# Optimization experiments

Hardware: AMD Instinct MI355X
Metric: run time of the kernel (lower is better)

Reference implementation:

```python
import jax, jax.numpy as jnp
import numpy as np

TEMPERATURE = 0.07
NUM_UNIFY_CLASSES = 256


def setup_inputs() -> dict:
    key = jax.random.key(0)
    k1, k2, k3 = jax.random.split(key, 3)
    b, c, h, w = 16, 256, 128, 128
    # small-magnitude feats so exp(logits) stays finite at temperature 0.07
    feats = jax.random.normal(k1, (b, c, h, w), dtype=jnp.float32) * 0.05
    queue = jax.random.normal(k2, (NUM_UNIFY_CLASSES, c), dtype=jnp.float32)
    queue = queue / jnp.linalg.norm(queue, axis=1, keepdims=True)  # unit rows, as a memory bank would hold
    labels = jax.random.randint(k3, (b * h * w, NUM_UNIFY_CLASSES), 0, 2, dtype=jnp.int32)
    return {"feats": feats, "queue": queue, "labels": labels}


def reference(feats, queue, labels):
    b, c, h, w = feats.shape
    # [b,c,h,w] -> [N, c]
    f = jnp.transpose(feats, (0, 2, 3, 1)).reshape(-1, c)
    # [N, M] logits
    logits = (f @ queue.T) / TEMPERATURE
    pos_mask = labels.reshape(-1, NUM_UNIFY_CLASSES).astype(logits.dtype)
    neg_mask = 1.0 - pos_mask
    sum_neg = jnp.sum(jnp.exp(logits) * neg_mask, axis=1)   # [N]
    sum_pos = jnp.sum(jnp.exp(-logits) * pos_mask, axis=1)  # [N]
    loss = jnp.log(sum_neg * sum_pos + 1.0)                 # [N]
    lb_num = jnp.sum(loss != 0)
    return jnp.where(lb_num == 0, jnp.float32(0.0),
                     jnp.sum(loss) / jnp.maximum(lb_num, 1).astype(loss.dtype))
```

## Files before the change

### kernel.cpp

```cpp
#include <hip/hip_runtime.h>
#include <hip/hip_bf16.h>


typedef __bf16 bf16x8 __attribute__((ext_vector_type(8)));
typedef float floatx4 __attribute__((ext_vector_type(4)));

using gl_void = const __attribute__((address_space(1))) void;
using lds_void = __attribute__((address_space(3))) void;

union BFrag {
  unsigned int u32[4];
  bf16x8 bf;
};

__device__ __forceinline__ unsigned int pack_bf2(float a, float b) {
  unsigned int ua = __float_as_uint(a) + 0x8000u;
  unsigned int ub = __float_as_uint(b) + 0x8000u;
  return (ua >> 16) | (ub & 0xffff0000u);
}

__global__ void qprep(const float* __restrict__ queue,
                      unsigned short* __restrict__ qs,
                      float* __restrict__ accum) {
  const int gt = blockIdx.x * 256 + threadIdx.x;
  const int t = gt >> 6;
  const int lane = gt & 63;
  const int m = ((t >> 3) << 4) | (lane & 15);
  const int k0 = ((t & 7) << 5) | ((lane >> 4) << 3);
  const float* qr = queue + m * 256 + k0;
  const float TINV = 14.2857142857142857f;
  BFrag u;
#pragma unroll
  for (int j = 0; j < 4; ++j)
    u.u32[j] = pack_bf2(qr[2 * j] * TINV, qr[2 * j + 1] * TINV);
  *(uint4*)(qs + (size_t)gt * 8) = *(const uint4*)u.u32;
  if (gt == 0) { accum[0] = 0.0f; accum[1] = 0.0f; }
}

__global__ __launch_bounds__(256, 2) void pcl_main(
    const float* __restrict__ feats,
    const int* __restrict__ labels,
    const unsigned short* __restrict__ qs,
    float* __restrict__ accum) {
  __shared__ float Fl[16640];
  __shared__ float Red[8][64];

  const int bx = blockIdx.x;
  const int bidx = bx >> 8;
  const int hw0 = (bx & 255) << 6;
  const int tid = threadIdx.x;
  const int w = tid >> 6;
  const int lane = tid & 63;
  const int qd = lane >> 4;
  const int s = lane & 15;

  {
    const float* gbase = feats + (size_t)bidx * 256 * 16384 + hw0;
#pragma unroll
    for (int i = 0; i < 16; ++i) {
      const int g = (w << 4) + i;
      const float* gp = gbase + (size_t)((g << 2) + qd) * 16384 + (s << 2);
      float* lp = &Fl[g * 260];
      __builtin_amdgcn_global_load_lds((gl_void*)gp, (lds_void*)lp, 16, 0, 0);
    }
  }

  floatx4 acc[4][4];
#pragma unroll
  for (int mt = 0; mt < 4; ++mt)
#pragma unroll
    for (int nt = 0; nt < 4; ++nt)
      acc[mt][nt] = floatx4{0.0f, 0.0f, 0.0f, 0.0f};

  __syncthreads();

  const bf16x8* qfrag = (const bf16x8*)qs;
#pragma unroll
  for (int ks = 0; ks < 8; ++ks) {
    bf16x8 af[4];
#pragma unroll
    for (int mt = 0; mt < 4; ++mt) {
      const int t = ((((w << 2) + mt) << 3) | ks);
      af[mt] = qfrag[t * 64 + lane];
    }
    bf16x8 bfv[4];
#pragma unroll
    for (int nt = 0; nt < 4; ++nt) {
      const float* bp = &Fl[((ks << 3) + (qd << 1)) * 260 + (nt << 4) + s];
      BFrag u;
      u.u32[0] = pack_bf2(bp[0], bp[64]);
      u.u32[1] = pack_bf2(bp[128], bp[192]);
      u.u32[2] = pack_bf2(bp[260], bp[324]);
      u.u32[3] = pack_bf2(bp[388], bp[452]);
      bfv[nt] = u.bf;
    }
#pragma unroll
    for (int mt = 0; mt < 4; ++mt)
#pragma unroll
      for (int nt = 0; nt < 4; ++nt)
        acc[mt][nt] = __builtin_amdgcn_mfma_f32_16x16x32_bf16(af[mt], bfv[nt],
                                                              acc[mt][nt], 0, 0, 0);
  }

  const size_t nbase = (size_t)bx << 6;
  int4 lab[4][4];
#pragma unroll
  for (int mt = 0; mt < 4; ++mt)
#pragma unroll
    for (int nt = 0; nt < 4; ++nt)
      lab[mt][nt] = *(const int4*)(labels + ((nbase + (nt << 4) + s) << 8) +
                                   (w << 6) + (mt << 4) + (qd << 2));

  float nn[4] = {0.f, 0.f, 0.f, 0.f};
  float pp[4] = {0.f, 0.f, 0.f, 0.f};
#define ACCUM_TERM(LV, AV)                          \
  do {                                              \
    const float fl_ = (float)(LV);                  \
    const float l_ = (AV);                          \
    const float e_ = __expf(l_);                    \
    const float en_ = __expf(-l_);                  \
    nn[nt] += (1.0f - fl_) * e_;                    \
    pp[nt] += fl_ * en_;                            \
  } while (0)

#pragma unroll
  for (int mt = 0; mt < 4; ++mt) {
#pragma unroll
    for (int nt = 0; nt < 4; ++nt) {
      const int4 lb = lab[mt][nt];
      const floatx4 a = acc[mt][nt];
      ACCUM_TERM(lb.x, a[0]);
      ACCUM_TERM(lb.y, a[1]);
      ACCUM_TERM(lb.z, a[2]);
      ACCUM_TERM(lb.w, a[3]);
    }
  }
#undef ACCUM_TERM

#pragma unroll
  for (int nt = 0; nt < 4; ++nt) {
    nn[nt] += __shfl_xor(nn[nt], 16);
    nn[nt] += __shfl_xor(nn[nt], 32);
    pp[nt] += __shfl_xor(pp[nt], 16);
    pp[nt] += __shfl_xor(pp[nt], 32);
  }
  if (lane < 16) {
#pragma unroll
    for (int nt = 0; nt < 4; ++nt) {
      Red[(w << 1) | 0][(nt << 4) + lane] = nn[nt];
      Red[(w << 1) | 1][(nt << 4) + lane] = pp[nt];
    }
  }
  __syncthreads();

  if (tid < 64) {
    const float sn = Red[0][tid] + Red[2][tid] + Red[4][tid] + Red[6][tid];
    const float sp = Red[1][tid] + Red[3][tid] + Red[5][tid] + Red[7][tid];
    float loss = logf(sn * sp + 1.0f);
    float c = (loss != 0.0f) ? 1.0f : 0.0f;
#pragma unroll
    for (int off = 32; off > 0; off >>= 1) {
      loss += __shfl_xor(loss, off);
      c += __shfl_xor(c, off);
    }
    if (tid == 0) {
      atomicAdd(&accum[0], loss);
      atomicAdd(&accum[1], c);
    }
  }
}

__global__ void pcl_finalize(const float* __restrict__ accum,
                             float* __restrict__ out) {
  const float ssum = accum[0];
  const float c = accum[1];
  out[0] = (c != 0.0f) ? (ssum / c) : 0.0f;
}

extern "C" void kernel_launch(void* const* d_in, const int* in_sizes, int n_in,
                              void* d_out, int out_size, void* d_ws, size_t ws_size,
                              hipStream_t stream) {
  (void)in_sizes; (void)n_in; (void)out_size; (void)ws_size;
  const float* feats = (const float*)d_in[0];
  const float* queue = (const float*)d_in[1];
  const int* labels = (const int*)d_in[2];

  unsigned short* qs = (unsigned short*)d_ws;
  float* accum = (float*)((char*)d_ws + 256 * 256 * sizeof(unsigned short));

  qprep<<<32, 256, 0, stream>>>(queue, qs, accum);
  pcl_main<<<4096, 256, 0, stream>>>(feats, labels, qs, accum);
  pcl_finalize<<<1, 1, 0, stream>>>(accum, (float*)d_out);
}
```

Measured before the change: 535.3 us.

## Convert feats to bf16 fragments at load, use exp2 with sign flip, raise occupancy

Feature tiles are now read from global with plain loads and packed into bf16 MFMA fragments once, into a 32KB LDS buffer, instead of staging fp32 via global_load_lds and repacking in the K loop. The queue is prescaled by log2(e)/T so the epilogue computes a single exp2 per logit, with the sign flipped by the label bit instead of two exps. Label loads are moved into the per-mt loop to cut register pressure, and launch bounds are raised to 4 blocks per SM. The trade-off is that strided scalar global loads replace the async LDS copy, and the lower register budget may cause spills.

```diff
diff --git a/kernel.cpp b/kernel.cpp
--- a/kernel.cpp
+++ b/kernel.cpp
@@ -5,11 +5,9 @@
 typedef __bf16 bf16x8 __attribute__((ext_vector_type(8)));
 typedef float floatx4 __attribute__((ext_vector_type(4)));
 
-using gl_void = const __attribute__((address_space(1))) void;
-using lds_void = __attribute__((address_space(3))) void;
-
 union BFrag {
   unsigned int u32[4];
+  uint4 v;
   bf16x8 bf;
 };
 
@@ -28,21 +26,21 @@
   const int m = ((t >> 3) << 4) | (lane & 15);
   const int k0 = ((t & 7) << 5) | ((lane >> 4) << 3);
   const float* qr = queue + m * 256 + k0;
-  const float TINV = 14.2857142857142857f;
+  const float SCALE = 20.6099291556f;
   BFrag u;
 #pragma unroll
   for (int j = 0; j < 4; ++j)
-    u.u32[j] = pack_bf2(qr[2 * j] * TINV, qr[2 * j + 1] * TINV);
-  *(uint4*)(qs + (size_t)gt * 8) = *(const uint4*)u.u32;
+    u.u32[j] = pack_bf2(qr[2 * j] * SCALE, qr[2 * j + 1] * SCALE);
+  *(uint4*)(qs + (size_t)gt * 8) = u.v;
   if (gt == 0) { accum[0] = 0.0f; accum[1] = 0.0f; }
 }
 
-__global__ __launch_bounds__(256, 2) void pcl_main(
+__global__ __launch_bounds__(256, 4) void pcl_main(
     const float* __restrict__ feats,
     const int* __restrict__ labels,
     const unsigned short* __restrict__ qs,
     float* __restrict__ accum) {
-  __shared__ float Fl[16640];
+  __shared__ uint4 Bf[2048];
   __shared__ float Red[8][64];
 
   const int bx = blockIdx.x;
@@ -55,13 +53,29 @@
   const int s = lane & 15;
 
   {
-    const float* gbase = feats + (size_t)bidx * 256 * 16384 + hw0;
+    const float* gbase = feats + (size_t)bidx * (256 * 16384) + hw0;
 #pragma unroll
-    for (int i = 0; i < 16; ++i) {
-      const int g = (w << 4) + i;
-      const float* gp = gbase + (size_t)((g << 2) + qd) * 16384 + (s << 2);
-      float* lp = &Fl[g * 260];
-      __builtin_amdgcn_global_load_lds((gl_void*)gp, (lds_void*)lp, 16, 0, 0);
+    for (int O2 = 0; O2 < 2; ++O2) {
+      const int O = (w << 1) + O2;
+      const int o = (O << 2) + qd;
+#pragma unroll
+      for (int N = 0; N < 4; ++N) {
+        const float* gp = gbase + (size_t)(o << 3) * 16384 + (N << 4) + s;
+        float v0 = gp[0];
+        float v1 = gp[16384];
+        float v2 = gp[2 * 16384];
+        float v3 = gp[3 * 16384];
+        float v4 = gp[4 * 16384];
+        float v5 = gp[5 * 16384];
+        float v6 = gp[6 * 16384];
+        float v7 = gp[7 * 16384];
+        BFrag u;
+        u.u32[0] = pack_bf2(v0, v1);
+        u.u32[1] = pack_bf2(v2, v3);
+        u.u32[2] = pack_bf2(v4, v5);
+        u.u32[3] = pack_bf2(v6, v7);
+        Bf[((O << 2) + N) * 64 + lane] = u.v;
+      }
     }
   }
 
@@ -75,6 +89,7 @@
   __syncthreads();
 
   const bf16x8* qfrag = (const bf16x8*)qs;
+  const bf16x8* bfrag = (const bf16x8*)Bf;
 #pragma unroll
   for (int ks = 0; ks < 8; ++ks) {
     bf16x8 af[4];
@@ -85,15 +100,8 @@
     }
     bf16x8 bfv[4];
 #pragma unroll
-    for (int nt = 0; nt < 4; ++nt) {
-      const float* bp = &Fl[((ks << 3) + (qd << 1)) * 260 + (nt << 4) + s];
-      BFrag u;
-      u.u32[0] = pack_bf2(bp[0], bp[64]);
-      u.u32[1] = pack_bf2(bp[128], bp[192]);
-      u.u32[2] = pack_bf2(bp[260], bp[324]);
-      u.u32[3] = pack_bf2(bp[388], bp[452]);
-      bfv[nt] = u.bf;
-    }
+    for (int nt = 0; nt < 4; ++nt)
+      bfv[nt] = bfrag[((ks << 2) + nt) * 64 + lane];
 #pragma unroll
     for (int mt = 0; mt < 4; ++mt)
 #pragma unroll
@@ -103,31 +111,28 @@
   }
 
   const size_t nbase = (size_t)bx << 6;
-  int4 lab[4][4];
-#pragma unroll
-  for (int mt = 0; mt < 4; ++mt)
-#pragma unroll
-    for (int nt = 0; nt < 4; ++nt)
-      lab[mt][nt] = *(const int4*)(labels + ((nbase + (nt << 4) + s) << 8) +
-                                   (w << 6) + (mt << 4) + (qd << 2));
 
   float nn[4] = {0.f, 0.f, 0.f, 0.f};
   float pp[4] = {0.f, 0.f, 0.f, 0.f};
-#define ACCUM_TERM(LV, AV)                          \
-  do {                                              \
-    const float fl_ = (float)(LV);                  \
-    const float l_ = (AV);                          \
-    const float e_ = __expf(l_);                    \
-    const float en_ = __expf(-l_);                  \
-    nn[nt] += (1.0f - fl_) * e_;                    \
-    pp[nt] += fl_ * en_;                            \
+#define ACCUM_TERM(LV, AV)                                                \
+  do {                                                                    \
+    const unsigned int y_ = (unsigned int)(LV);                           \
+    const float x_ = __uint_as_float(__float_as_uint(AV) ^ (y_ << 31));   \
+    const float e_ = exp2f(x_);                                           \
+    nn[nt] += y_ ? 0.0f : e_;                                             \
+    pp[nt] += y_ ? e_ : 0.0f;                                             \
   } while (0)
 
 #pragma unroll
   for (int mt = 0; mt < 4; ++mt) {
+    int4 lab[4];
+#pragma unroll
+    for (int nt = 0; nt < 4; ++nt)
+      lab[nt] = *(const int4*)(labels + ((nbase + (nt << 4) + s) << 8) +
+                               (w << 6) + (mt << 4) + (qd << 2));
 #pragma unroll
     for (int nt = 0; nt < 4; ++nt) {
-      const int4 lb = lab[mt][nt];
+      const int4 lb = lab[nt];
       const floatx4 a = acc[mt][nt];
       ACCUM_TERM(lb.x, a[0]);
       ACCUM_TERM(lb.y, a[1]);
```

Result: no change. 541.4 us (+1.2%).
